# Performance work log

Measured on AMD Instinct MI355X. Metric: run time of the kernel, lower is better.

The kernel has to match this reference:

```python
import jax, jax.numpy as jnp
import numpy as np
from jax import lax

K = 3
STRIDE = 2
PADDING = 1
OUTPUT_PADDING = 1


def setup_inputs() -> dict:
    key = jax.random.key(0)
    k1, k2, k3, k4 = jax.random.split(key, 4)
    B, C, H, W = 4, 64, 128, 128
    outC = 64
    g_ch = 3
    x = jax.random.normal(k1, (B, C, H, W), dtype=jnp.float32)
    guide = jax.random.normal(k2, (B, g_ch, H * STRIDE, W * STRIDE), dtype=jnp.float32)
    # kaiming-uniform-like init scale: bound = 1/sqrt(fan_in), fan_in = C*K*K
    fan_in = C * K * K
    bound = 1.0 / np.sqrt(fan_in)
    weight = jax.random.uniform(k3, (C, outC, K, K), dtype=jnp.float32, minval=-bound, maxval=bound)
    bias = jax.random.uniform(k4, (outC,), dtype=jnp.float32, minval=-bound, maxval=bound)
    return {"x": x, "guide": guide, "weight": weight, "bias": bias}


def _patches(t, pad):
    # torch.nn.functional.unfold equivalent: channel ordering (C, kh, kw)
    return lax.conv_general_dilated_patches(
        t, filter_shape=(K, K), window_strides=(1, 1), padding=[(pad, pad), (pad, pad)]
    )


def reference(x, guide, weight, bias):
    B, C, H, W = x.shape
    _, g_ch, GH, GW = guide.shape
    s, p, op = STRIDE, PADDING, OUTPUT_PADDING

    # Gaussian affinity kernel from guide patches
    gp = (K - 1) // 2
    guide_unf = _patches(guide, gp).reshape(B, g_ch, K * K, GH, GW)
    diff = guide_unf - guide_unf[:, :, K * K // 2 : K * K // 2 + 1]
    kern = jnp.exp(-0.5 * jnp.sum(diff * diff, axis=1))  # [B, K*K, GH, GW]
    kern = kern.reshape(B, 1, K, K, GH, GW)

    # depthwise transposed conv with all-ones 1x1 kernel == zero-stuffing upsample
    Ht, Wt = (H - 1) * s + 1, (W - 1) * s + 1
    temp = jnp.zeros((B, C, Ht, Wt), dtype=x.dtype).at[:, :, ::s, ::s].set(x)
    pad = (K - 1) - p
    temp = jnp.pad(temp, ((0, 0), (0, 0), (pad, pad + op), (pad, pad + op)))

    cols = _patches(temp, 0).reshape(B, C, K, K, GH, GW)
    in_mul_k = cols * kern  # [B, C, K, K, GH, GW]
    out = jnp.einsum("bcklhw,cokl->bohw", in_mul_k, weight)
    return out + bias.reshape(1, -1, 1, 1)
```

## Files before the change

kernel.cpp:

```cpp
#include <hip/hip_runtime.h>
#include <math.h>

typedef __attribute__((ext_vector_type(8))) short short8;
typedef __attribute__((ext_vector_type(4))) float float4v;

#define GH_ 256
#define GW_ 256
#define H_  128
#define W_  128
#define C_  64
#define OC_ 64
#define NB_ 4

static __device__ __forceinline__ unsigned short f2bf(float f) {
    union { float f; unsigned int u; } v; v.f = f;
    unsigned int u = v.u;
    unsigned int r = u + 0x7FFFu + ((u >> 16) & 1u);
    return (unsigned short)(r >> 16);
}

static __device__ __forceinline__ int swz(int byte) {
    return byte ^ (((byte >> 7) & 7) << 4);
}

__global__ __launch_bounds__(512) void prep_w(const float* __restrict__ w,
                                              unsigned short* __restrict__ wtb) {
    const int t = blockIdx.x;
    const int kh = t / 3, kw = t - kh * 3;
    for (int i = threadIdx.x; i < OC_ * C_; i += 512) {
        int c = i & 63, o = (i >> 6) & 63;
        wtb[t * OC_ * C_ + i] = f2bf(w[((c * OC_ + o) * 3 + kh) * 3 + kw]);
    }
}

__global__ __launch_bounds__(512, 4) void pac_fused(
    const float* __restrict__ x,
    const float* __restrict__ guide,
    const unsigned short* __restrict__ wtb,
    const float* __restrict__ bias,
    float* __restrict__ out)
{
    __shared__ unsigned short xt[3 * 128 * 64];
    __shared__ float xaux[64 * 33];

    const int ypair = blockIdx.x;
    const int b     = blockIdx.y;
    const int hp    = blockIdx.z;
    const int tid   = threadIdx.x;
    const int R0    = ypair * 2;
    const int nrows = 2 + hp;

    {
        float (*xl)[33] = (float (*)[33])xaux;
        const int c = tid >> 3, f4 = tid & 7;
        for (int lr = 0; lr < nrows; ++lr) {
            int srow = R0 + lr; if (srow > H_ - 1) srow = H_ - 1;
            const float* xrow = x + (((size_t)(b * C_ + c) * H_) + srow) * W_;
            for (int qtr = 0; qtr < 4; ++qtr) {
                const int iw0 = qtr * 32;
                float4 rd = *(const float4*)(xrow + iw0 + f4 * 4);
                xl[c][f4 * 4 + 0] = rd.x;
                xl[c][f4 * 4 + 1] = rd.y;
                xl[c][f4 * 4 + 2] = rd.z;
                xl[c][f4 * 4 + 3] = rd.w;
                __syncthreads();
                #pragma unroll
                for (int j = 0; j < 2; ++j) {
                    int jj = tid + j * 512;
                    int cl = jj >> 5, cp = jj & 31;
                    unsigned int lo = f2bf(xl[2 * cp][cl]);
                    unsigned int hi = f2bf(xl[2 * cp + 1][cl]);
                    int lin = ((lr * 128 + iw0 + cl) << 7) + cp * 4;
                    *(unsigned int*)((char*)xt + swz(lin)) = lo | (hi << 16);
                }
                __syncthreads();
            }
        }
    }

    const int ntr = 1 + hp;
    const int nslot = 3 * ntr;
    float (*klds)[2][128] = (float (*)[2][128])xaux;

    for (int i = tid; i < nslot * 256; i += 512) {
        int px = i & 255, slot = i >> 8;
        int py = px >> 7, xp = px & 127;
        int wp, r, q;
        if (slot < ntr) { wp = 0; r = slot; q = 0; }
        else { int s = slot - ntr; wp = 1; r = s >> 1; q = s & 1; }
        int yp = R0 + py;
        int h = 2 * yp + hp, w = 2 * xp + wp;
        int rr = yp + r, cl = xp + q;
        float kv = 0.f;
        if (rr < H_ && cl < W_) {
            int hh = rr * 2, ww = cl * 2;
            const float* gb = guide + (size_t)b * 3 * GH_ * GW_;
            float s2 = 0.f;
            #pragma unroll
            for (int g = 0; g < 3; ++g) {
                float d = gb[(g * GH_ + hh) * GW_ + ww] - gb[(g * GH_ + h) * GW_ + w];
                s2 += d * d;
            }
            kv = __expf(-0.5f * s2);
        }
        klds[slot][py][xp] = kv;
    }
    __syncthreads();

    const int wave = tid >> 6, lane = tid & 63;
    const int l16 = lane & 15, qk = lane >> 4;
    const int oh  = wave & 1;
    const int py  = (wave >> 1) & 1;
    const int xh  = wave >> 2;
    const int obase = oh * 32;
    const int xpb   = xh * 64;
    const int yp = R0 + py;
    const int h  = 2 * yp + hp;

    for (int mf = 0; mf < 2; ++mf) {
        float acc0[4][4];
        float acc1[4][4];
        #pragma unroll
        for (int nf = 0; nf < 4; ++nf)
            #pragma unroll
            for (int e = 0; e < 4; ++e) { acc0[nf][e] = 0.f; acc1[nf][e] = 0.f; }

        const int o = obase + mf * 16 + l16;

        for (int r = 0; r <= hp; ++r) {
            int kh = hp ? 2 * r : 1;
            int rowc = yp + r; if (rowc > H_ - 1) rowc = H_ - 1;
            int lr0 = rowc - R0;
            int s_c = r;
            int s_l = ntr + 2 * r;
            int s_r = ntr + 2 * r + 1;

            short8 af[3][2];
            #pragma unroll
            for (int kw3 = 0; kw3 < 3; ++kw3) {
                const short8* wbase = (const short8*)(wtb + (size_t)(kh * 3 + kw3) * OC_ * C_);
                af[kw3][0] = wbase[(o * C_ + qk * 8) >> 3];
                af[kw3][1] = wbase[(o * C_ + 32 + qk * 8) >> 3];
            }

            #pragma unroll
            for (int nf = 0; nf < 4; ++nf) {
                int xp = xpb + nf * 16 + l16;
                int col1 = xp + 1; if (col1 > W_ - 1) col1 = W_ - 1;
                int base0 = ((lr0 * 128 + xp)   << 7) + qk * 16;
                int base1 = ((lr0 * 128 + col1) << 7) + qk * 16;
                short8 b0a = *(const short8*)((const char*)xt + swz(base0));
                short8 b0b = *(const short8*)((const char*)xt + swz(base0 + 64));
                short8 b1a = *(const short8*)((const char*)xt + swz(base1));
                short8 b1b = *(const short8*)((const char*)xt + swz(base1 + 64));
                float kc = klds[s_c][py][xp];
                float kl = klds[s_l][py][xp];
                float kr = klds[s_r][py][xp];
                float4v d;
                d = (float4v){0.f, 0.f, 0.f, 0.f};
                d = __builtin_amdgcn_mfma_f32_16x16x32_bf16(af[1][0], b0a, d, 0, 0, 0);
                d = __builtin_amdgcn_mfma_f32_16x16x32_bf16(af[1][1], b0b, d, 0, 0, 0);
                #pragma unroll
                for (int e = 0; e < 4; ++e) acc0[nf][e] += kc * d[e];
                d = (float4v){0.f, 0.f, 0.f, 0.f};
                d = __builtin_amdgcn_mfma_f32_16x16x32_bf16(af[0][0], b0a, d, 0, 0, 0);
                d = __builtin_amdgcn_mfma_f32_16x16x32_bf16(af[0][1], b0b, d, 0, 0, 0);
                #pragma unroll
                for (int e = 0; e < 4; ++e) acc1[nf][e] += kl * d[e];
                d = (float4v){0.f, 0.f, 0.f, 0.f};
                d = __builtin_amdgcn_mfma_f32_16x16x32_bf16(af[2][0], b1a, d, 0, 0, 0);
                d = __builtin_amdgcn_mfma_f32_16x16x32_bf16(af[2][1], b1b, d, 0, 0, 0);
                #pragma unroll
                for (int e = 0; e < 4; ++e) acc1[nf][e] += kr * d[e];
            }
        }

        float bv[4];
        #pragma unroll
        for (int e = 0; e < 4; ++e)
            bv[e] = bias[obase + mf * 16 + qk * 4 + e];

        #pragma unroll
        for (int e = 0; e < 4; ++e) {
            int oo = obase + mf * 16 + qk * 4 + e;
            float2* op = (float2*)(out + (((size_t)b * OC_ + oo) * GH_ + h) * GW_);
            #pragma unroll
            for (int nf = 0; nf < 4; ++nf) {
                int xp = xpb + nf * 16 + l16;
                float2 v;
                v.x = acc0[nf][e] + bv[e];
                v.y = acc1[nf][e] + bv[e];
                op[xp] = v;
            }
        }
    }
}

extern "C" void kernel_launch(void* const* d_in, const int* in_sizes, int n_in,
                              void* d_out, int out_size, void* d_ws, size_t ws_size,
                              hipStream_t stream) {
    const float* x     = (const float*)d_in[0];
    const float* guide = (const float*)d_in[1];
    const float* wgt   = (const float*)d_in[2];
    const float* bias  = (const float*)d_in[3];
    float* out = (float*)d_out;

    unsigned short* wtb = (unsigned short*)d_ws;

    prep_w<<<dim3(9), 512, 0, stream>>>(wgt, wtb);
    pac_fused<<<dim3(64, 4, 2), 512, 0, stream>>>(x, guide, wtb, bias, out);
}
```

Before: 106.2 us.

## Merge both output row parities into one 1024-thread block sharing staged input

Folds the two row-parity blocks (the blockIdx.z split) into a single 1024-thread block, with waves 8-15 handling the odd parity. The staged bf16 input tile and all nine affinity slots are built once per block instead of being duplicated across two blocks. The input staging is rewritten so each thread loads eight channels of one column directly, converts them and writes a 16-byte swizzled LDS store, which removes the transpose buffer and its per-quarter barriers. In exchange there are half as many blocks, and the 1024-thread blocks with an unchanged occupancy hint of 4 may put more pressure on registers and occupancy.

```diff
diff --git a/kernel.cpp b/kernel.cpp
--- a/kernel.cpp
+++ b/kernel.cpp
@@ -3,6 +3,7 @@
 
 typedef __attribute__((ext_vector_type(8))) short short8;
 typedef __attribute__((ext_vector_type(4))) float float4v;
+typedef __attribute__((ext_vector_type(4))) unsigned int uint4v;
 
 #define GH_ 256
 #define GW_ 256
@@ -33,7 +34,7 @@
     }
 }
 
-__global__ __launch_bounds__(512, 4) void pac_fused(
+__global__ __launch_bounds__(1024, 4) void pac_fused(
     const float* __restrict__ x,
     const float* __restrict__ guide,
     const unsigned short* __restrict__ wtb,
@@ -41,55 +42,43 @@
     float* __restrict__ out)
 {
     __shared__ unsigned short xt[3 * 128 * 64];
-    __shared__ float xaux[64 * 33];
+    __shared__ float klds[9][2][128];
 
     const int ypair = blockIdx.x;
     const int b     = blockIdx.y;
-    const int hp    = blockIdx.z;
     const int tid   = threadIdx.x;
     const int R0    = ypair * 2;
-    const int nrows = 2 + hp;
 
     {
-        float (*xl)[33] = (float (*)[33])xaux;
-        const int c = tid >> 3, f4 = tid & 7;
-        for (int lr = 0; lr < nrows; ++lr) {
+        const int col = tid & 127;
+        const int cg  = tid >> 7;
+        #pragma unroll
+        for (int lr = 0; lr < 3; ++lr) {
             int srow = R0 + lr; if (srow > H_ - 1) srow = H_ - 1;
-            const float* xrow = x + (((size_t)(b * C_ + c) * H_) + srow) * W_;
-            for (int qtr = 0; qtr < 4; ++qtr) {
-                const int iw0 = qtr * 32;
-                float4 rd = *(const float4*)(xrow + iw0 + f4 * 4);
-                xl[c][f4 * 4 + 0] = rd.x;
-                xl[c][f4 * 4 + 1] = rd.y;
-                xl[c][f4 * 4 + 2] = rd.z;
-                xl[c][f4 * 4 + 3] = rd.w;
-                __syncthreads();
-                #pragma unroll
-                for (int j = 0; j < 2; ++j) {
-                    int jj = tid + j * 512;
-                    int cl = jj >> 5, cp = jj & 31;
-                    unsigned int lo = f2bf(xl[2 * cp][cl]);
-                    unsigned int hi = f2bf(xl[2 * cp + 1][cl]);
-                    int lin = ((lr * 128 + iw0 + cl) << 7) + cp * 4;
-                    *(unsigned int*)((char*)xt + swz(lin)) = lo | (hi << 16);
-                }
-                __syncthreads();
-            }
-        }
-    }
-
-    const int ntr = 1 + hp;
-    const int nslot = 3 * ntr;
-    float (*klds)[2][128] = (float (*)[2][128])xaux;
-
-    for (int i = tid; i < nslot * 256; i += 512) {
-        int px = i & 255, slot = i >> 8;
+            const float* xs = x + (((size_t)(b * C_ + cg * 8) * H_) + srow) * W_ + col;
+            float v[8];
+            #pragma unroll
+            for (int j = 0; j < 8; ++j) v[j] = xs[(size_t)j * H_ * W_];
+            unsigned int p0 = (unsigned int)f2bf(v[0]) | ((unsigned int)f2bf(v[1]) << 16);
+            unsigned int p1 = (unsigned int)f2bf(v[2]) | ((unsigned int)f2bf(v[3]) << 16);
+            unsigned int p2 = (unsigned int)f2bf(v[4]) | ((unsigned int)f2bf(v[5]) << 16);
+            unsigned int p3 = (unsigned int)f2bf(v[6]) | ((unsigned int)f2bf(v[7]) << 16);
+            int byte = ((lr * 128 + col) << 7) + cg * 16;
+            *(uint4v*)((char*)xt + swz(byte)) = (uint4v){p0, p1, p2, p3};
+        }
+    }
+
+    for (int i = tid; i < 9 * 256; i += 1024) {
+        int px = i & 255, gs = i >> 8;
         int py = px >> 7, xp = px & 127;
+        int lhp = (gs < 3) ? 0 : 1;
+        int ls  = (gs < 3) ? gs : gs - 3;
+        int lntr = 1 + lhp;
         int wp, r, q;
-        if (slot < ntr) { wp = 0; r = slot; q = 0; }
-        else { int s = slot - ntr; wp = 1; r = s >> 1; q = s & 1; }
+        if (ls < lntr) { wp = 0; r = ls; q = 0; }
+        else { int s = ls - lntr; wp = 1; r = s >> 1; q = s & 1; }
         int yp = R0 + py;
-        int h = 2 * yp + hp, w = 2 * xp + wp;
+        int h = 2 * yp + lhp, w = 2 * xp + wp;
         int rr = yp + r, cl = xp + q;
         float kv = 0.f;
         if (rr < H_ && cl < W_) {
@@ -103,7 +92,7 @@
             }
             kv = __expf(-0.5f * s2);
         }
-        klds[slot][py][xp] = kv;
+        klds[gs][py][xp] = kv;
     }
     __syncthreads();
 
@@ -111,11 +100,14 @@
     const int l16 = lane & 15, qk = lane >> 4;
     const int oh  = wave & 1;
     const int py  = (wave >> 1) & 1;
-    const int xh  = wave >> 2;
+    const int xh  = (wave >> 2) & 1;
+    const int hp  = wave >> 3;
     const int obase = oh * 32;
     const int xpb   = xh * 64;
     const int yp = R0 + py;
     const int h  = 2 * yp + hp;
+    const int ntr = 1 + hp;
+    const int kbase = hp ? 3 : 0;
 
     for (int mf = 0; mf < 2; ++mf) {
         float acc0[4][4];
@@ -131,9 +123,9 @@
             int kh = hp ? 2 * r : 1;
             int rowc = yp + r; if (rowc > H_ - 1) rowc = H_ - 1;
             int lr0 = rowc - R0;
-            int s_c = r;
-            int s_l = ntr + 2 * r;
-            int s_r = ntr + 2 * r + 1;
+            int s_c = kbase + r;
+            int s_l = kbase + ntr + 2 * r;
+            int s_r = kbase + ntr + 2 * r + 1;
 
             short8 af[3][2];
             #pragma unroll
@@ -208,5 +200,5 @@
     unsigned short* wtb = (unsigned short*)d_ws;
 
     prep_w<<<dim3(9), 512, 0, stream>>>(wgt, wtb);
-    pac_fused<<<dim3(64, 4, 2), 512, 0, stream>>>(x, guide, wtb, bias, out);
-}
+    pac_fused<<<dim3(64, 4), 1024, 0, stream>>>(x, guide, wtb, bias, out);
+}
```

Result: faster. 103.4 us (median of 2 runs) (-2.6%).
